# Kernel optimization log

Measured on AMD Instinct MI355X. Metric: run time of the kernel, lower is better.

## Reference

```python
import jax, jax.numpy as jnp
import numpy as np

CTX_LEN = 2048
DK = 128
SEQ = 8192


def setup_inputs() -> dict:
    key = jax.random.key(0)
    kx, kq, kk, kv = jax.random.split(key, 4)
    x = jax.random.normal(kx, (SEQ, CTX_LEN), dtype=jnp.float32)
    # module initializes weights as rand(ctxLen, dk) * 0.05
    wq = jax.random.uniform(kq, (CTX_LEN, DK), dtype=jnp.float32) * 0.05
    wk = jax.random.uniform(kk, (CTX_LEN, DK), dtype=jnp.float32) * 0.05
    wv = jax.random.uniform(kv, (CTX_LEN, DK), dtype=jnp.float32) * 0.05
    return {"x": x, "wq": wq, "wk": wk, "wv": wv}


def reference(x, wq, wk, wv):
    dk = wq.shape[1]
    q = x @ wq          # [S, dk]
    k = x @ wk          # [S, dk]
    v = x @ wv          # [S, dk]
    # NOTE: source multiplies by sqrt(dk) (not the usual divide)
    scores = jnp.einsum("sd,td->st", q, k) * jnp.sqrt(jnp.float32(dk))  # [S, S]
    # NOTE: source softmax over dim=0 (column-wise)
    attn = jax.nn.softmax(scores, axis=0)
    return attn @ v     # [S, dk]
```

## Files before the change

kernel.cpp:

```cpp
#include <hip/hip_runtime.h>
#include <stdint.h>

#define SEQ 8192
#define CTX 2048
#define DK  128

typedef __attribute__((ext_vector_type(8))) __bf16 bf16x8;
typedef __attribute__((ext_vector_type(4))) float f32x4;
typedef unsigned short u16;

__device__ __forceinline__ u16 f2bf(float f) {
  unsigned int u = __builtin_bit_cast(unsigned int, f);
  u += 0x7FFFu + ((u >> 16) & 1u);
  return (u16)(u >> 16);
}
__device__ __forceinline__ u16 f2bf_fast(float f) {
  unsigned int u = __builtin_bit_cast(unsigned int, f);
  return (u16)((u + 0x8000u) >> 16);
}
__device__ __forceinline__ float bf2f(u16 h) {
  unsigned int u = ((unsigned int)h) << 16;
  return __builtin_bit_cast(float, u);
}
__device__ __forceinline__ void gl_lds16(const void* g, void* l) {
  __builtin_amdgcn_global_load_lds((__attribute__((address_space(1))) void*)g,
                                   (__attribute__((address_space(3))) void*)l, 16, 0, 0);
}
__device__ __forceinline__ f32x4 mfma16(bf16x8 a, bf16x8 b, f32x4 c) {
  return __builtin_amdgcn_mfma_f32_16x16x32_bf16(a, b, c, 0, 0, 0);
}

__global__ __launch_bounds__(256) void k_cvt_x(const float* __restrict__ x, u16* __restrict__ xb) {
  int i = blockIdx.x * 256 + threadIdx.x;
  float4 a = ((const float4*)x)[i];
  ushort4 r;
  r.x = f2bf(a.x); r.y = f2bf(a.y); r.z = f2bf(a.z); r.w = f2bf(a.w);
  ((ushort4*)xb)[i] = r;
}

__global__ __launch_bounds__(256) void k_cvt_w(const float* __restrict__ wq, const float* __restrict__ wk,
                                               const float* __restrict__ wv, u16* __restrict__ wT) {
  int mat = blockIdx.y;
  const float* w = mat == 0 ? wq : (mat == 1 ? wk : wv);
  float scale = (mat == 0) ? 11.313708498984761f : 1.0f;
  int tk = blockIdx.x & 63, tn = blockIdx.x >> 6;
  __shared__ float t[32][33];
  int tx = threadIdx.x & 31, ty = threadIdx.x >> 5;
  int k0 = tk * 32, n0 = tn * 32;
#pragma unroll
  for (int j = 0; j < 4; j++) {
    int kk = ty + j * 8;
    t[kk][tx] = w[(size_t)(k0 + kk) * DK + n0 + tx] * scale;
  }
  __syncthreads();
  u16* o = wT + (size_t)mat * DK * CTX;
#pragma unroll
  for (int j = 0; j < 4; j++) {
    int nn = ty + j * 8;
    o[(size_t)(n0 + nn) * CTX + k0 + tx] = f2bf(t[tx][nn]);
  }
}

__global__ __launch_bounds__(256, 2) void k_qkv(const u16* __restrict__ xb, const u16* __restrict__ wT,
                                                u16* __restrict__ qb, u16* __restrict__ kb, u16* __restrict__ vb) {
  __shared__ __align__(16) u16 As[128 * 32];
  __shared__ __align__(16) u16 Bs[128 * 32];
  int bid = blockIdx.x;
  int xcd = bid & 7, j = bid >> 3;
  int mat = j % 3, mb = xcd * 8 + j / 3;
  const u16* B = wT + (size_t)mat * DK * CTX;
  u16* C = mat == 0 ? qb : (mat == 1 ? kb : vb);
  int tid = threadIdx.x, lane = tid & 63, w = tid >> 6;
  int r15 = lane & 15, gq = lane >> 4;
  int wr = w >> 1, wc = w & 1;
  f32x4 acc[4][4] = {};
  for (int k0 = 0; k0 < CTX; k0 += 32) {
    __syncthreads();
#pragma unroll
    for (int i = 0; i < 2; i++) {
      int c = i * 256 + tid; int row = c >> 2, cc = c & 3;
      gl_lds16(xb + (size_t)(mb * 128 + row) * CTX + k0 + cc * 8, &As[(i * 256 + w * 64) * 8]);
    }
#pragma unroll
    for (int i = 0; i < 2; i++) {
      int c = i * 256 + tid; int row = c >> 2, cc = c & 3;
      gl_lds16(B + (size_t)row * CTX + k0 + cc * 8, &Bs[(i * 256 + w * 64) * 8]);
    }
    asm volatile("s_waitcnt vmcnt(0)" ::: "memory");
    __syncthreads();
    bf16x8 af[4], bfr[4];
#pragma unroll
    for (int mi = 0; mi < 4; mi++) af[mi] = *(const bf16x8*)&As[(wr * 64 + mi * 16 + r15) * 32 + gq * 8];
#pragma unroll
    for (int ni = 0; ni < 4; ni++) bfr[ni] = *(const bf16x8*)&Bs[(wc * 64 + ni * 16 + r15) * 32 + gq * 8];
#pragma unroll
    for (int mi = 0; mi < 4; mi++)
#pragma unroll
      for (int ni = 0; ni < 4; ni++)
        acc[mi][ni] = mfma16(af[mi], bfr[ni], acc[mi][ni]);
  }
#pragma unroll
  for (int mi = 0; mi < 4; mi++)
#pragma unroll
    for (int ni = 0; ni < 4; ni++)
#pragma unroll
      for (int rr = 0; rr < 4; rr++) {
        int mrow = mb * 128 + wr * 64 + mi * 16 + gq * 4 + rr;
        int ncol = wc * 64 + ni * 16 + r15;
        C[(size_t)mrow * DK + ncol] = f2bf(acc[mi][ni][rr]);
      }
}

__global__ __launch_bounds__(256, 2) void k_p2(const u16* __restrict__ qb, const u16* __restrict__ kb,
                                               float* __restrict__ m_part, float* __restrict__ z_part) {
  __shared__ __align__(16) u16 Ks2[4 * 128 * 32];
  __shared__ __align__(16) u16 Qs2[4 * 64 * 32];
  const float L2E = 1.4426950408889634f;
  int bid = blockIdx.x;
  int ss = bid & 7, tb = bid >> 3;
  int t0 = tb * 128, s0 = ss * 1024;
  int tid = threadIdx.x, lane = tid & 63, w = tid >> 6;
  int r15 = lane & 15, gq = lane >> 4;
#pragma unroll
  for (int i = 0; i < 8; i++) {
    int c = i * 256 + tid; int kd = c >> 9, row = (c >> 2) & 127, cc = c & 3;
    gl_lds16(kb + (size_t)(t0 + row) * DK + kd * 32 + cc * 8, &Ks2[(i * 256 + w * 64) * 8]);
  }
  asm volatile("s_waitcnt vmcnt(0)" ::: "memory");
  __syncthreads();
  bf16x8 af[2][4];
#pragma unroll
  for (int mi = 0; mi < 2; mi++)
#pragma unroll
    for (int kd = 0; kd < 4; kd++)
      af[mi][kd] = *(const bf16x8*)&Ks2[kd * 4096 + (w * 32 + mi * 16 + r15) * 32 + gq * 8];
  float runM[8], runZ[8];
#pragma unroll
  for (int jj = 0; jj < 8; jj++) { runM[jj] = -3.0e38f; runZ[jj] = 0.f; }

  for (int sc = 0; sc < 1024; sc += 64) {
#pragma unroll
    for (int i = 0; i < 4; i++) {
      int c = i * 256 + tid; int kd = c >> 8, row = (c >> 2) & 63, cc = c & 3;
      gl_lds16(qb + (size_t)(s0 + sc + row) * DK + kd * 32 + cc * 8, &Qs2[(i * 256 + w * 64) * 8]);
    }
    asm volatile("s_waitcnt vmcnt(0)" ::: "memory");
    __syncthreads();
    f32x4 pacc[4][2] = {};
#pragma unroll
    for (int ni = 0; ni < 4; ni++)
#pragma unroll
      for (int kd = 0; kd < 4; kd++) {
        bf16x8 bq = *(const bf16x8*)&Qs2[kd * 2048 + (ni * 16 + r15) * 32 + gq * 8];
        pacc[ni][0] = mfma16(af[0][kd], bq, pacc[ni][0]);
        pacc[ni][1] = mfma16(af[1][kd], bq, pacc[ni][1]);
      }
    __syncthreads();
#pragma unroll
    for (int mi = 0; mi < 2; mi++)
#pragma unroll
      for (int rr = 0; rr < 4; rr++) {
        int jj = mi * 4 + rr;
        float m8 = fmaxf(fmaxf(pacc[0][mi][rr], pacc[1][mi][rr]),
                         fmaxf(pacc[2][mi][rr], pacc[3][mi][rr])) * L2E;
        if (m8 > runM[jj] - 60.f) {
          float nm = fmaxf(runM[jj], m8);
          float z = runZ[jj] * __builtin_amdgcn_exp2f(runM[jj] - nm);
#pragma unroll
          for (int ni = 0; ni < 4; ni++)
            z += __builtin_amdgcn_exp2f(fmaf(pacc[ni][mi][rr], L2E, -nm));
          runZ[jj] = z; runM[jj] = nm;
        }
      }
  }
#pragma unroll
  for (int d = 1; d < 16; d <<= 1) {
#pragma unroll
    for (int jj = 0; jj < 8; jj++) {
      float oM = __shfl_xor(runM[jj], d);
      float oZ = __shfl_xor(runZ[jj], d);
      float nm = fmaxf(runM[jj], oM);
      runZ[jj] = runZ[jj] * __builtin_amdgcn_exp2f(runM[jj] - nm) + oZ * __builtin_amdgcn_exp2f(oM - nm);
      runM[jj] = nm;
    }
  }
  if (r15 == 0) {
#pragma unroll
    for (int mi = 0; mi < 2; mi++)
#pragma unroll
      for (int rr = 0; rr < 4; rr++) {
        int t = t0 + w * 32 + mi * 16 + gq * 4 + rr;
        m_part[ss * SEQ + t] = runM[mi * 4 + rr];
        z_part[ss * SEQ + t] = runZ[mi * 4 + rr];
      }
  }
}

__global__ __launch_bounds__(256) void k_p2c(const float* __restrict__ m_part, const float* __restrict__ z_part,
                                             const u16* __restrict__ vb, float* __restrict__ mL,
                                             u16* __restrict__ vT) {
  int t0 = blockIdx.x * 64;
  int tid = threadIdx.x;
  __shared__ float rz[64];
  __shared__ __align__(16) u16 vt[64 * DK];
  if (tid < 64) {
    int t = t0 + tid;
    float m0 = -3.0e38f, z = 0.f;
#pragma unroll
    for (int p = 0; p < 8; p++) {
      float a = m_part[p * SEQ + t], b = z_part[p * SEQ + t];
      float nm = fmaxf(m0, a);
      z = z * __builtin_amdgcn_exp2f(m0 - nm) + b * __builtin_amdgcn_exp2f(a - nm);
      m0 = nm;
    }
    mL[t] = m0;
    rz[tid] = 1.0f / z;
  }
  const uint4* vs = (const uint4*)(vb + (size_t)t0 * DK);
  uint4* vd = (uint4*)vt;
#pragma unroll
  for (int i = 0; i < 4; i++) vd[i * 256 + tid] = vs[i * 256 + tid];
  __syncthreads();
  int d = tid >> 1, half = tid & 1;
#pragma unroll
  for (int jj = 0; jj < 32; jj++) {
    int tl = half * 32 + jj;
    float f = bf2f(vt[tl * DK + d]) * rz[tl];
    vT[(size_t)d * SEQ + t0 + tl] = f2bf(f);
  }
}

__global__ __launch_bounds__(256, 2) void k_p3(const u16* __restrict__ qb, const u16* __restrict__ kb,
                                               const u16* __restrict__ vT, const float* __restrict__ mLg,
                                               float* __restrict__ outp) {
  __shared__ __align__(16) u16 Ks2[4 * 64 * 32];
  __shared__ __align__(16) u16 Vs2[2 * 128 * 32];
  __shared__ __align__(16) u16 Ps[2 * 128 * 40];
  __shared__ __align__(16) float mLs[1024];
  const float L2E = 1.4426950408889634f;
  int bid = blockIdx.x;
  int ts = bid & 7, sb = bid >> 3;
  int s0 = sb * 128, tbase = ts * 1024;
  int tid = threadIdx.x, lane = tid & 63, w = tid >> 6;
  int r15 = lane & 15, gq = lane >> 4;
  int wr = w >> 1, wc = w & 1;
  gl_lds16(mLg + tbase + tid * 4, &mLs[w * 256]);
  bf16x8 qf[2][4];
#pragma unroll
  for (int ni = 0; ni < 2; ni++)
#pragma unroll
    for (int kd = 0; kd < 4; kd++)
      qf[ni][kd] = *(const bf16x8*)(qb + (size_t)(s0 + w * 32 + ni * 16 + r15) * DK + kd * 32 + gq * 8);
  f32x4 o[4][4] = {};
  for (int tc = 0; tc < 1024; tc += 64) {
    __syncthreads();
#pragma unroll
    for (int i = 0; i < 4; i++) {
      int c = i * 256 + tid; int kd = c >> 8, t = (c >> 2) & 63, cc = c & 3;
      gl_lds16(kb + (size_t)(tbase + tc + t) * DK + kd * 32 + cc * 8, &Ks2[(i * 256 + w * 64) * 8]);
    }
#pragma unroll
    for (int i = 0; i < 4; i++) {
      int c = i * 256 + tid; int kt = c >> 9, d = (c >> 2) & 127, cc = c & 3;
      gl_lds16(vT + (size_t)d * SEQ + tbase + tc + kt * 32 + cc * 8, &Vs2[(i * 256 + w * 64) * 8]);
    }
    asm volatile("s_waitcnt vmcnt(0)" ::: "memory");
    __syncthreads();
#pragma unroll
    for (int mi = 0; mi < 4; mi++) {
      bf16x8 a4[4];
#pragma unroll
      for (int kd = 0; kd < 4; kd++)
        a4[kd] = *(const bf16x8*)&Ks2[kd * 2048 + (mi * 16 + r15) * 32 + gq * 8];
      f32x4 p0 = {}, p1 = {};
#pragma unroll
      for (int kd = 0; kd < 4; kd++) {
        p0 = mfma16(a4[kd], qf[0][kd], p0);
        p1 = mfma16(a4[kd], qf[1][kd], p1);
      }
      ushort4 pk0, pk1;
      {
        float e;
        float mv0 = mLs[tc + mi * 16 + gq * 4 + 0];
        float mv1 = mLs[tc + mi * 16 + gq * 4 + 1];
        float mv2 = mLs[tc + mi * 16 + gq * 4 + 2];
        float mv3 = mLs[tc + mi * 16 + gq * 4 + 3];
        e = __builtin_amdgcn_exp2f(fmaf(p0[0], L2E, -mv0)); pk0.x = f2bf_fast(e);
        e = __builtin_amdgcn_exp2f(fmaf(p0[1], L2E, -mv1)); pk0.y = f2bf_fast(e);
        e = __builtin_amdgcn_exp2f(fmaf(p0[2], L2E, -mv2)); pk0.z = f2bf_fast(e);
        e = __builtin_amdgcn_exp2f(fmaf(p0[3], L2E, -mv3)); pk0.w = f2bf_fast(e);
        e = __builtin_amdgcn_exp2f(fmaf(p1[0], L2E, -mv0)); pk1.x = f2bf_fast(e);
        e = __builtin_amdgcn_exp2f(fmaf(p1[1], L2E, -mv1)); pk1.y = f2bf_fast(e);
        e = __builtin_amdgcn_exp2f(fmaf(p1[2], L2E, -mv2)); pk1.z = f2bf_fast(e);
        e = __builtin_amdgcn_exp2f(fmaf(p1[3], L2E, -mv3)); pk1.w = f2bf_fast(e);
      }
      int ktp = mi >> 1;
      int w32 = (mi & 1) * 16 + gq * 4;
      *(ushort4*)&Ps[ktp * 5120 + (w * 32 + r15) * 40 + w32] = pk0;
      *(ushort4*)&Ps[ktp * 5120 + (w * 32 + 16 + r15) * 40 + w32] = pk1;
    }
    __syncthreads();
#pragma unroll
    for (int kt = 0; kt < 2; kt++) {
      bf16x8 pa[4], vv[4];
#pragma unroll
      for (int mi2 = 0; mi2 < 4; mi2++)
        pa[mi2] = *(const bf16x8*)&Ps[kt * 5120 + (wr * 64 + mi2 * 16 + r15) * 40 + gq * 8];
#pragma unroll
      for (int ni2 = 0; ni2 < 4; ni2++)
        vv[ni2] = *(const bf16x8*)&Vs2[kt * 4096 + (wc * 64 + ni2 * 16 + r15) * 32 + gq * 8];
#pragma unroll
      for (int mi2 = 0; mi2 < 4; mi2++)
#pragma unroll
        for (int ni2 = 0; ni2 < 4; ni2++)
          o[mi2][ni2] = mfma16(pa[mi2], vv[ni2], o[mi2][ni2]);
    }
  }
  float* dst = outp + (size_t)ts * SEQ * DK;
#pragma unroll
  for (int mi2 = 0; mi2 < 4; mi2++)
#pragma unroll
    for (int ni2 = 0; ni2 < 4; ni2++)
#pragma unroll
      for (int rr = 0; rr < 4; rr++) {
        int srow = s0 + wr * 64 + mi2 * 16 + gq * 4 + rr;
        int dcol = wc * 64 + ni2 * 16 + r15;
        dst[(size_t)srow * DK + dcol] = o[mi2][ni2][rr];
      }
}

__global__ __launch_bounds__(256) void k_p4(const float* __restrict__ outp, float* __restrict__ out) {
  int i = blockIdx.x * 256 + threadIdx.x;
  const float4* s = (const float4*)outp;
  float4 a = s[i];
#pragma unroll
  for (int p = 1; p < 8; p++) {
    float4 b = s[(size_t)p * 262144 + i];
    a.x += b.x; a.y += b.y; a.z += b.z; a.w += b.w;
  }
  ((float4*)out)[i] = a;
}

extern "C" void kernel_launch(void* const* d_in, const int* in_sizes, int n_in,
                              void* d_out, int out_size, void* d_ws, size_t ws_size,
                              hipStream_t stream) {
  (void)in_sizes; (void)n_in; (void)out_size; (void)ws_size;
  const float* x  = (const float*)d_in[0];
  const float* wq = (const float*)d_in[1];
  const float* wk = (const float*)d_in[2];
  const float* wv = (const float*)d_in[3];
  float* out = (float*)d_out;

  char* wsb = (char*)d_ws;
  u16*   xb    = (u16*)wsb;
  float* outp  = (float*)wsb;
  u16*   wT    = (u16*)(wsb + 33554432);
  u16*   qb    = (u16*)(wsb + 35127296);
  u16*   kb    = (u16*)(wsb + 37224448);
  u16*   vb    = (u16*)(wsb + 39321600);
  u16*   vT    = (u16*)(wsb + 41418752);
  float* mLf   = (float*)(wsb + 43515904);
  float* mpart = (float*)(wsb + 43548672);
  float* zpart = (float*)(wsb + 43810816);

  k_cvt_x<<<16384, 256, 0, stream>>>(x, xb);
  k_cvt_w<<<dim3(256, 3), 256, 0, stream>>>(wq, wk, wv, wT);
  k_qkv<<<192, 256, 0, stream>>>(xb, wT, qb, kb, vb);
  k_p2<<<512, 256, 0, stream>>>(qb, kb, mpart, zpart);
  k_p2c<<<128, 256, 0, stream>>>(mpart, zpart, vb, mLf, vT);
  k_p3<<<512, 256, 0, stream>>>(qb, kb, vT, mLf, outp);
  k_p4<<<1024, 256, 0, stream>>>(outp, out);
}
```

Measured before the change: 222.6 us.

## Double-buffer LDS tiles with XOR swizzle across QKV, stats and output kernels

Adds double-buffered LDS staging so the next global-to-LDS tile load is issued before the current tile's MFMA work in the QKV GEMM, the row-statistics pass and the P·V pass. The QKV k-step is doubled to 64, which halves the number of barriers. An XOR swizzle on the 16-byte chunk index is applied to both LDS writes and fragment reads to reduce bank conflicts. The per-column max values in k_p3 are now read straight from global memory into registers instead of through shared memory. The cost is more LDS per block, which may limit occupancy at two blocks per CU, plus extra address arithmetic.

```diff
diff --git a/kernel.cpp b/kernel.cpp
--- a/kernel.cpp
+++ b/kernel.cpp
@@ -63,8 +63,8 @@
 
 __global__ __launch_bounds__(256, 2) void k_qkv(const u16* __restrict__ xb, const u16* __restrict__ wT,
                                                 u16* __restrict__ qb, u16* __restrict__ kb, u16* __restrict__ vb) {
-  __shared__ __align__(16) u16 As[128 * 32];
-  __shared__ __align__(16) u16 Bs[128 * 32];
+  __shared__ __align__(16) u16 As[2][8192];
+  __shared__ __align__(16) u16 Bs[2][8192];
   int bid = blockIdx.x;
   int xcd = bid & 7, j = bid >> 3;
   int mat = j % 3, mb = xcd * 8 + j / 3;
@@ -73,31 +73,50 @@
   int tid = threadIdx.x, lane = tid & 63, w = tid >> 6;
   int r15 = lane & 15, gq = lane >> 4;
   int wr = w >> 1, wc = w & 1;
+  int gqx = gq ^ ((r15 >> 1) & 3);
+
+  auto stage = [&](int buf, int k0) {
+#pragma unroll
+    for (int i = 0; i < 4; i++) {
+      int c = i * 256 + tid;
+      int kd = c >> 9, row = (c >> 2) & 127, cc = (c & 3) ^ ((c >> 3) & 3);
+      gl_lds16(xb + (size_t)(mb * 128 + row) * CTX + k0 + kd * 32 + cc * 8, &As[buf][(i * 256 + w * 64) * 8]);
+    }
+#pragma unroll
+    for (int i = 0; i < 4; i++) {
+      int c = i * 256 + tid;
+      int kd = c >> 9, row = (c >> 2) & 127, cc = (c & 3) ^ ((c >> 3) & 3);
+      gl_lds16(B + (size_t)row * CTX + k0 + kd * 32 + cc * 8, &Bs[buf][(i * 256 + w * 64) * 8]);
+    }
+  };
+
   f32x4 acc[4][4] = {};
-  for (int k0 = 0; k0 < CTX; k0 += 32) {
-    __syncthreads();
-#pragma unroll
-    for (int i = 0; i < 2; i++) {
-      int c = i * 256 + tid; int row = c >> 2, cc = c & 3;
-      gl_lds16(xb + (size_t)(mb * 128 + row) * CTX + k0 + cc * 8, &As[(i * 256 + w * 64) * 8]);
-    }
-#pragma unroll
-    for (int i = 0; i < 2; i++) {
-      int c = i * 256 + tid; int row = c >> 2, cc = c & 3;
-      gl_lds16(B + (size_t)row * CTX + k0 + cc * 8, &Bs[(i * 256 + w * 64) * 8]);
-    }
+  stage(0, 0);
+  asm volatile("s_waitcnt vmcnt(0)" ::: "memory");
+  __syncthreads();
+  for (int it = 0; it < 32; ++it) {
+    int buf = it & 1;
+    if (it < 31) stage(buf ^ 1, it * 64 + 64);
+    bf16x8 af[2][4], bfr[2][4];
+#pragma unroll
+    for (int kd = 0; kd < 2; kd++)
+#pragma unroll
+      for (int mi = 0; mi < 4; mi++)
+        af[kd][mi] = *(const bf16x8*)&As[buf][kd * 4096 + (wr * 64 + mi * 16 + r15) * 32 + gqx * 8];
+#pragma unroll
+    for (int kd = 0; kd < 2; kd++)
+#pragma unroll
+      for (int ni = 0; ni < 4; ni++)
+        bfr[kd][ni] = *(const bf16x8*)&Bs[buf][kd * 4096 + (wc * 64 + ni * 16 + r15) * 32 + gqx * 8];
+#pragma unroll
+    for (int mi = 0; mi < 4; mi++)
+#pragma unroll
+      for (int ni = 0; ni < 4; ni++) {
+        acc[mi][ni] = mfma16(af[0][mi], bfr[0][ni], acc[mi][ni]);
+        acc[mi][ni] = mfma16(af[1][mi], bfr[1][ni], acc[mi][ni]);
+      }
     asm volatile("s_waitcnt vmcnt(0)" ::: "memory");
     __syncthreads();
-    bf16x8 af[4], bfr[4];
-#pragma unroll
-    for (int mi = 0; mi < 4; mi++) af[mi] = *(const bf16x8*)&As[(wr * 64 + mi * 16 + r15) * 32 + gq * 8];
-#pragma unroll
-    for (int ni = 0; ni < 4; ni++) bfr[ni] = *(const bf16x8*)&Bs[(wc * 64 + ni * 16 + r15) * 32 + gq * 8];
-#pragma unroll
-    for (int mi = 0; mi < 4; mi++)
-#pragma unroll
-      for (int ni = 0; ni < 4; ni++)
-        acc[mi][ni] = mfma16(af[mi], bfr[ni], acc[mi][ni]);
   }
 #pragma unroll
   for (int mi = 0; mi < 4; mi++)
@@ -113,19 +132,32 @@
 
 __global__ __launch_bounds__(256, 2) void k_p2(const u16* __restrict__ qb, const u16* __restrict__ kb,
                                                float* __restrict__ m_part, float* __restrict__ z_part) {
-  __shared__ __align__(16) u16 Ks2[4 * 128 * 32];
-  __shared__ __align__(16) u16 Qs2[4 * 64 * 32];
+  __shared__ __align__(16) u16 Ks2[16384];
+  __shared__ __align__(16) u16 Qs2[2][8192];
   const float L2E = 1.4426950408889634f;
   int bid = blockIdx.x;
   int ss = bid & 7, tb = bid >> 3;
   int t0 = tb * 128, s0 = ss * 1024;
   int tid = threadIdx.x, lane = tid & 63, w = tid >> 6;
   int r15 = lane & 15, gq = lane >> 4;
+  int gqx = gq ^ ((r15 >> 1) & 3);
+
+  auto stageQ = [&](int buf, int sc) {
+#pragma unroll
+    for (int i = 0; i < 4; i++) {
+      int c = i * 256 + tid;
+      int kd = c >> 8, row = (c >> 2) & 63, cc = (c & 3) ^ ((c >> 3) & 3);
+      gl_lds16(qb + (size_t)(s0 + sc + row) * DK + kd * 32 + cc * 8, &Qs2[buf][(i * 256 + w * 64) * 8]);
+    }
+  };
+
 #pragma unroll
   for (int i = 0; i < 8; i++) {
-    int c = i * 256 + tid; int kd = c >> 9, row = (c >> 2) & 127, cc = c & 3;
+    int c = i * 256 + tid;
+    int kd = c >> 9, row = (c >> 2) & 127, cc = (c & 3) ^ ((c >> 3) & 3);
     gl_lds16(kb + (size_t)(t0 + row) * DK + kd * 32 + cc * 8, &Ks2[(i * 256 + w * 64) * 8]);
   }
+  stageQ(0, 0);
   asm volatile("s_waitcnt vmcnt(0)" ::: "memory");
   __syncthreads();
   bf16x8 af[2][4];
@@ -133,29 +165,23 @@
   for (int mi = 0; mi < 2; mi++)
 #pragma unroll
     for (int kd = 0; kd < 4; kd++)
-      af[mi][kd] = *(const bf16x8*)&Ks2[kd * 4096 + (w * 32 + mi * 16 + r15) * 32 + gq * 8];
+      af[mi][kd] = *(const bf16x8*)&Ks2[kd * 4096 + (w * 32 + mi * 16 + r15) * 32 + gqx * 8];
   float runM[8], runZ[8];
 #pragma unroll
   for (int jj = 0; jj < 8; jj++) { runM[jj] = -3.0e38f; runZ[jj] = 0.f; }
 
   for (int sc = 0; sc < 1024; sc += 64) {
-#pragma unroll
-    for (int i = 0; i < 4; i++) {
-      int c = i * 256 + tid; int kd = c >> 8, row = (c >> 2) & 63, cc = c & 3;
-      gl_lds16(qb + (size_t)(s0 + sc + row) * DK + kd * 32 + cc * 8, &Qs2[(i * 256 + w * 64) * 8]);
-    }
-    asm volatile("s_waitcnt vmcnt(0)" ::: "memory");
-    __syncthreads();
+    int buf = (sc >> 6) & 1;
+    if (sc < 960) stageQ(buf ^ 1, sc + 64);
     f32x4 pacc[4][2] = {};
 #pragma unroll
     for (int ni = 0; ni < 4; ni++)
 #pragma unroll
       for (int kd = 0; kd < 4; kd++) {
-        bf16x8 bq = *(const bf16x8*)&Qs2[kd * 2048 + (ni * 16 + r15) * 32 + gq * 8];
+        bf16x8 bq = *(const bf16x8*)&Qs2[buf][kd * 2048 + (ni * 16 + r15) * 32 + gqx * 8];
         pacc[ni][0] = mfma16(af[0][kd], bq, pacc[ni][0]);
         pacc[ni][1] = mfma16(af[1][kd], bq, pacc[ni][1]);
       }
-    __syncthreads();
 #pragma unroll
     for (int mi = 0; mi < 2; mi++)
 #pragma unroll
@@ -172,6 +198,8 @@
           runZ[jj] = z; runM[jj] = nm;
         }
       }
+    asm volatile("s_waitcnt vmcnt(0)" ::: "memory");
+    __syncthreads();
   }
 #pragma unroll
   for (int d = 1; d < 16; d <<= 1) {
@@ -233,10 +261,9 @@
 __global__ __launch_bounds__(256, 2) void k_p3(const u16* __restrict__ qb, const u16* __restrict__ kb,
                                                const u16* __restrict__ vT, const float* __restrict__ mLg,
                                                float* __restrict__ outp) {
-  __shared__ __align__(16) u16 Ks2[4 * 64 * 32];
-  __shared__ __align__(16) u16 Vs2[2 * 128 * 32];
+  __shared__ __align__(16) u16 Ks2[8192];
+  __shared__ __align__(16) u16 Vs2[2][8192];
   __shared__ __align__(16) u16 Ps[2 * 128 * 40];
-  __shared__ __align__(16) float mLs[1024];
   const float L2E = 1.4426950408889634f;
   int bid = blockIdx.x;
   int ts = bid & 7, sb = bid >> 3;
@@ -244,34 +271,50 @@
   int tid = threadIdx.x, lane = tid & 63, w = tid >> 6;
   int r15 = lane & 15, gq = lane >> 4;
   int wr = w >> 1, wc = w & 1;
-  gl_lds16(mLg + tbase + tid * 4, &mLs[w * 256]);
+  int gqx = gq ^ ((r15 >> 1) & 3);
+
+  auto stageK = [&](int tc) {
+#pragma unroll
+    for (int i = 0; i < 4; i++) {
+      int c = i * 256 + tid;
+      int kd = c >> 8, t = (c >> 2) & 63, cc = (c & 3) ^ ((c >> 3) & 3);
+      gl_lds16(kb + (size_t)(tbase + tc + t) * DK + kd * 32 + cc * 8, &Ks2[(i * 256 + w * 64) * 8]);
+    }
+  };
+  auto stageV = [&](int buf, int tc) {
+#pragma unroll
+    for (int i = 0; i < 4; i++) {
+      int c = i * 256 + tid;
+      int kt = c >> 9, d = (c >> 2) & 127, cc = (c & 3) ^ ((c >> 3) & 3);
+      gl_lds16(vT + (size_t)d * SEQ + tbase + tc + kt * 32 + cc * 8, &Vs2[buf][(i * 256 + w * 64) * 8]);
+    }
+  };
+
   bf16x8 qf[2][4];
 #pragma unroll
   for (int ni = 0; ni < 2; ni++)
 #pragma unroll
     for (int kd = 0; kd < 4; kd++)
       qf[ni][kd] = *(const bf16x8*)(qb + (size_t)(s0 + w * 32 + ni * 16 + r15) * DK + kd * 32 + gq * 8);
+
+  stageK(0);
+  stageV(0, 0);
+  asm volatile("s_waitcnt vmcnt(0)" ::: "memory");
+  __syncthreads();
+
   f32x4 o[4][4] = {};
   for (int tc = 0; tc < 1024; tc += 64) {
-    __syncthreads();
-#pragma unroll
-    for (int i = 0; i < 4; i++) {
-      int c = i * 256 + tid; int kd = c >> 8, t = (c >> 2) & 63, cc = c & 3;
-      gl_lds16(kb + (size_t)(tbase + tc + t) * DK + kd * 32 + cc * 8, &Ks2[(i * 256 + w * 64) * 8]);
-    }
-#pragma unroll
-    for (int i = 0; i < 4; i++) {
-      int c = i * 256 + tid; int kt = c >> 9, d = (c >> 2) & 127, cc = c & 3;
-      gl_lds16(vT + (size_t)d * SEQ + tbase + tc + kt * 32 + cc * 8, &Vs2[(i * 256 + w * 64) * 8]);
-    }
-    asm volatile("s_waitcnt vmcnt(0)" ::: "memory");
-    __syncthreads();
+    int vbuf = (tc >> 6) & 1;
+    float4 mv4[4];
+#pragma unroll
+    for (int mi = 0; mi < 4; mi++)
+      mv4[mi] = *(const float4*)(mLg + tbase + tc + mi * 16 + gq * 4);
 #pragma unroll
     for (int mi = 0; mi < 4; mi++) {
       bf16x8 a4[4];
 #pragma unroll
       for (int kd = 0; kd < 4; kd++)
-        a4[kd] = *(const bf16x8*)&Ks2[kd * 2048 + (mi * 16 + r15) * 32 + gq * 8];
+        a4[kd] = *(const bf16x8*)&Ks2[kd * 2048 + (mi * 16 + r15) * 32 + gqx * 8];
       f32x4 p0 = {}, p1 = {};
 #pragma unroll
       for (int kd = 0; kd < 4; kd++) {
@@ -281,10 +324,7 @@
       ushort4 pk0, pk1;
       {
         float e;
-        float mv0 = mLs[tc + mi * 16 + gq * 4 + 0];
-        float mv1 = mLs[tc + mi * 16 + gq * 4 + 1];
-        float mv2 = mLs[tc + mi * 16 + gq * 4 + 2];
-        float mv3 = mLs[tc + mi * 16 + gq * 4 + 3];
+        float mv0 = mv4[mi].x, mv1 = mv4[mi].y, mv2 = mv4[mi].z, mv3 = mv4[mi].w;
         e = __builtin_amdgcn_exp2f(fmaf(p0[0], L2E, -mv0)); pk0.x = f2bf_fast(e);
         e = __builtin_amdgcn_exp2f(fmaf(p0[1], L2E, -mv1)); pk0.y = f2bf_fast(e);
         e = __builtin_amdgcn_exp2f(fmaf(p0[2], L2E, -mv2)); pk0.z = f2bf_fast(e);
@@ -300,6 +340,10 @@
       *(ushort4*)&Ps[ktp * 5120 + (w * 32 + 16 + r15) * 40 + w32] = pk1;
     }
     __syncthreads();
+    if (tc < 960) {
+      stageK(tc + 64);
+      stageV(vbuf ^ 1, tc + 64);
+    }
 #pragma unroll
     for (int kt = 0; kt < 2; kt++) {
       bf16x8 pa[4], vv[4];
@@ -308,13 +352,15 @@
         pa[mi2] = *(const bf16x8*)&Ps[kt * 5120 + (wr * 64 + mi2 * 16 + r15) * 40 + gq * 8];
 #pragma unroll
       for (int ni2 = 0; ni2 < 4; ni2++)
-        vv[ni2] = *(const bf16x8*)&Vs2[kt * 4096 + (wc * 64 + ni2 * 16 + r15) * 32 + gq * 8];
+        vv[ni2] = *(const bf16x8*)&Vs2[vbuf][kt * 4096 + (wc * 64 + ni2 * 16 + r15) * 32 + gqx * 8];
 #pragma unroll
       for (int mi2 = 0; mi2 < 4; mi2++)
 #pragma unroll
         for (int ni2 = 0; ni2 < 4; ni2++)
           o[mi2][ni2] = mfma16(pa[mi2], vv[ni2], o[mi2][ni2]);
     }
+    asm volatile("s_waitcnt vmcnt(0)" ::: "memory");
+    __syncthreads();
   }
   float* dst = outp + (size_t)ts * SEQ * DK;
 #pragma unroll
```

Result: faster. 217.1 us (-2.4%).
